# Kernel tuning notes

Measured on AMD Instinct MI355X. Metric: run time of the kernel, lower is better.

## Reference

```python
import jax, jax.numpy as jnp
import numpy as np

T1 = -0.075410217
T2 = 0.0
T3 = 0.062207676


def my_squash2(s_j):
    # s_j: [B, 1, C, O, 1]; piecewise-linear rescale based on sorted channel-0 magnitudes.
    B, _, C, O, _ = s_j.shape
    f = s_j[:, 0, :, 0, 0]                      # [B, C] first element of each capsule
    order = jnp.argsort(f, axis=1)
    srt = jnp.take_along_axis(f, order, axis=1)  # ascending sort per sample
    i1 = jnp.sum(srt < T1, axis=1, keepdims=True)
    i2 = jnp.sum(srt < T2, axis=1, keepdims=True)
    i3 = jnp.sum(srt < T3, axis=1, keepdims=True)
    pos = jnp.arange(C)[None, :]
    seg1 = -0.074520095 * srt + 0.349297946
    seg2 = -0.534473989 * srt + 0.27196494
    seg3 = 0.637642944 * srt + 0.295330779
    seg4 = 0.169344703 * srt + 0.353784456
    # faithful to torch slices [0:i1-1], [i1:i2-1], [i2:i3-1], [i3:9] (segment-end indices untouched)
    m1 = (i1 > 0) & (pos < i1 - 1)
    m2 = (i2 > 0) & (i2 > i1) & (pos >= i1) & (pos < i2 - 1)
    m3 = (i3 > 0) & (i3 > i2) & (pos >= i2) & (pos < i3 - 1)
    m4 = (i3 < C) & (pos >= i3) & (pos < C - 1)
    new_srt = jnp.where(m1, seg1, jnp.where(m2, seg2, jnp.where(m3, seg3, jnp.where(m4, seg4, srt))))
    inv = jnp.argsort(order, axis=1)
    new_f = jnp.take_along_axis(new_srt, inv, axis=1)  # unsort back to capsule order
    # torch code mutates s_j in place: channel 0 of each capsule becomes new_f
    s_mut = s_j.at[:, 0, :, 0, 0].set(new_f)
    scale = new_f[:, None, :, None, None]            # expanded over out_channels
    return scale * s_mut, s_mut


def setup_inputs() -> dict:
    key = jax.random.key(0)
    k0, k1, k2, k3 = jax.random.split(key, 4)
    B, R, C, O, I = 100, 1152, 10, 16, 8
    return {
        "x0": jax.random.normal(k0, (B, R, I), dtype=jnp.float32),
        "x1": jax.random.normal(k1, (B, R, I), dtype=jnp.float32),
        "x2": jax.random.normal(k2, (B, 1, 28, 28), dtype=jnp.float32),
        "W": jax.random.normal(k3, (1, R, C, O, I), dtype=jnp.float32),
        "train_or_test": 0,
        "epch": 0,
    }


def reference(x0, x1, x2, W, train_or_test, epch):
    B, R, I = x0.shape
    C, O = W.shape[2], W.shape[3]
    squashed_u = jnp.broadcast_to(x0[:, :, None, :, None], (B, R, C, I, 1))
    # u_hat[b,r,c,o] = sum_i W[0,r,c,o,i] * x0[b,r,i]
    u_hat = jnp.einsum('rcoi,bri->brco', W[0], x0)[..., None]  # [B,R,C,O,1]
    b_ij = jnp.zeros((1, R, C, 1), dtype=x0.dtype)
    num_iterations = 3
    for it in range(num_iterations):
        c_ij = jax.nn.softmax(b_ij, axis=1)                    # over routes
        c_full = jnp.broadcast_to(c_ij, (B, R, C, 1))[..., None]
        s_j = jnp.sum(c_full * u_hat, axis=1, keepdims=True)   # [B,1,C,O,1]
        v_j, s_mut = my_squash2(s_j)
        if it < num_iterations - 1:
            a = jnp.einsum('brco,bco->brc', u_hat[..., 0], v_j[:, 0, :, :, 0])
            b_ij = b_ij + jnp.mean(a, axis=0)[None, :, :, None]
    Wb = jnp.broadcast_to(W, (B,) + W.shape[1:])
    return (v_j[:, 0], c_full, Wb, squashed_u, x1, x2, s_mut[:, 0])
```

## Files before the change

### kernel.cpp

```cpp
#include <hip/hip_runtime.h>

#define B 100
#define R 1152
#define C 10
#define O 16
#define I 8
#define RI 9216
#define CO 160
#define RCHUNK 32
#define NRC 36
#define KCH (RCHUNK*I)

typedef float f4raw __attribute__((ext_vector_type(4)));
__device__ __forceinline__ void nt_store4(const float4& v, float4* p) {
    __builtin_nontemporal_store(*(const f4raw*)&v, (f4raw*)p);
}

#define WS_BCOL 0
#define WS_CSM  11520
#define WS_XT   23040
#define WS_PART 944768
#define WS_V    1520768
#define WS_SMUT 1536768

#define WB_OUT_BASE 292000
#define WB_WSTRIDE  368640
#define WB_NCHUNK   1440
#define WB_BG       20
#define WB_UNITS    7200

__device__ __forceinline__ void wb_unit(const float4* __restrict__ W4,
                                        float4* __restrict__ out, int unit) {
    int wchunk = unit % WB_NCHUNK;
    int bg = unit / WB_NCHUNK;
    int idx = wchunk * 256 + threadIdx.x;
    float4 v = W4[idx];
    float4* dst = out + WB_OUT_BASE + (size_t)bg * WB_BG * WB_WSTRIDE + idx;
    #pragma unroll
    for (int b = 0; b < WB_BG; b++) {
        nt_store4(v, dst);
        dst += WB_WSTRIDE;
    }
}

__global__ void k_init(const float* __restrict__ x0, float* __restrict__ ws,
                       const float4* __restrict__ W4, float4* __restrict__ out) {
    if (blockIdx.x >= 3600) { wb_unit(W4, out, 0 + (blockIdx.x - 3600)); return; }
    int idx = blockIdx.x * 256 + threadIdx.x;
    if (idx < RI * B) {
        int k = idx / B;
        int b = idx - k * B;
        ws[WS_XT + idx] = x0[b * RI + k];
    }
    if (idx < R * C) ws[WS_BCOL + idx] = 0.f;
}

__global__ __launch_bounds__(256) void k_gemm1(const float* __restrict__ Wg,
                                               float* __restrict__ ws,
                                               float4* __restrict__ out, int wbBase) {
    if (blockIdx.x >= NRC) {
        wb_unit((const float4*)Wg, out, wbBase + (blockIdx.x - NRC) + 90 * blockIdx.y);
        return;
    }
    const int rc = blockIdx.x, c = blockIdx.y;
    const int t = threadIdx.x;
    const int r0 = rc * RCHUNK;
    __shared__ float red[256];
    __shared__ float cw[RCHUNK];
    __shared__ float lw[KCH * O];
    const float* bcol = ws + WS_BCOL + c * R;

    float lm = -3.4e38f;
    for (int r = t; r < R; r += 256) lm = fmaxf(lm, bcol[r]);
    red[t] = lm; __syncthreads();
    for (int s = 128; s > 0; s >>= 1) { if (t < s) red[t] = fmaxf(red[t], red[t + s]); __syncthreads(); }
    const float m = red[0]; __syncthreads();
    float ls = 0.f;
    for (int r = t; r < R; r += 256) ls += expf(bcol[r] - m);
    red[t] = ls; __syncthreads();
    for (int s = 128; s > 0; s >>= 1) { if (t < s) red[t] += red[t + s]; __syncthreads(); }
    const float sinv = 1.f / red[0];
    if (t < RCHUNK) {
        float w_ = expf(bcol[r0 + t] - m) * sinv;
        cw[t] = w_;
        ws[WS_CSM + (r0 + t) * C + c] = w_;
    }
    __syncthreads();

    for (int j = t; j < KCH * O; j += 256) {
        int rr = j >> 7;
        int rem = j & 127;
        int o = rem >> 3, i = rem & 7;
        lw[(rr * I + i) * O + o] = cw[rr] * Wg[((size_t)(r0 + rr) * C + c) * (O * I) + rem];
    }
    __syncthreads();

    const int bl = t & 63, og = t >> 6;
    const float* xT = ws + WS_XT + (r0 * I) * B + bl;
    const float4* lw4 = (const float4*)lw;
    float4 a0 = {0, 0, 0, 0}, a1 = {0, 0, 0, 0};
    #pragma unroll 8
    for (int k = 0; k < KCH; k++) {
        float xv0 = xT[0];
        float xv1 = xT[64];
        float4 wv = lw4[k * 4 + og];
        a0.x += xv0 * wv.x; a0.y += xv0 * wv.y; a0.z += xv0 * wv.z; a0.w += xv0 * wv.w;
        a1.x += xv1 * wv.x; a1.y += xv1 * wv.y; a1.z += xv1 * wv.z; a1.w += xv1 * wv.w;
        xT += B;
    }
    float4* part4 = (float4*)(ws + WS_PART);
    int base = ((c * NRC + rc) * B + bl) * 4 + og;
    part4[base] = a0;
    if (bl < B - 64) part4[base + 64 * 4] = a1;
}

__global__ __launch_bounds__(256) void k_squash(float* __restrict__ ws,
                                                const float4* __restrict__ W4,
                                                float4* __restrict__ out, int wbBase) {
    if (blockIdx.x >= B) { wb_unit(W4, out, wbBase + (blockIdx.x - B)); return; }
    const int b = blockIdx.x, t = threadIdx.x;
    __shared__ float sl[CO];
    __shared__ float nf[C];
    if (t < CO) {
        int c = t >> 4, o = t & 15;
        float s = 0.f;
        const float* p = ws + WS_PART + ((size_t)c * NRC * B + b) * 16 + o;
        #pragma unroll
        for (int rc = 0; rc < NRC; rc++) s += p[(size_t)rc * B * 16];
        sl[t] = s;
    }
    __syncthreads();
    if (t < C) {
        float fv[C];
        #pragma unroll
        for (int c2 = 0; c2 < C; c2++) fv[c2] = sl[c2 * O];
        float mine = sl[t * O];
        int rank = 0, i1 = 0, i2 = 0, i3 = 0;
        #pragma unroll
        for (int c2 = 0; c2 < C; c2++) {
            rank += (fv[c2] < mine) || (fv[c2] == mine && c2 < t);
            i1 += fv[c2] < -0.075410217f;
            i2 += fv[c2] < 0.0f;
            i3 += fv[c2] < 0.062207676f;
        }
        float nv = mine;
        if (i1 > 0 && rank < i1 - 1)                               nv = -0.074520095f * mine + 0.349297946f;
        else if (i2 > 0 && i2 > i1 && rank >= i1 && rank < i2 - 1) nv = -0.534473989f * mine + 0.27196494f;
        else if (i3 > 0 && i3 > i2 && rank >= i2 && rank < i3 - 1) nv = 0.637642944f * mine + 0.295330779f;
        else if (i3 < C && rank >= i3 && rank < C - 1)             nv = 0.169344703f * mine + 0.353784456f;
        nf[t] = nv;
    }
    __syncthreads();
    if (t < CO) {
        int c = t >> 4, o = t & 15;
        float sv = sl[t];
        float nfv = nf[c];
        float smut = (o == 0) ? nfv : sv;
        ws[WS_SMUT + b * CO + t] = smut;
        ws[WS_V + b * CO + t] = nfv * smut;
    }
}

__global__ __launch_bounds__(256) void k_agree(const float* __restrict__ Wg,
                                               float* __restrict__ ws,
                                               float4* __restrict__ out, int wbBase) {
    if (blockIdx.x >= R) { wb_unit((const float4*)Wg, out, wbBase + (blockIdx.x - R)); return; }
    const int r = blockIdx.x, t = threadIdx.x;
    __shared__ float vt[32 * B];
    __shared__ float xs[I * B];
    __shared__ float arr[CO * I];
    for (int j = t; j < I * B; j += 256) xs[j] = ws[WS_XT + (size_t)r * I * B + j];
    const int i = t & 7, co0 = t >> 3;
    const float4* xs4 = (const float4*)(xs + i * B);
    const float4* vt4 = (const float4*)(vt + co0 * B);
    for (int ch = 0; ch < 5; ch++) {
        __syncthreads();
        for (int j = t; j < 32 * B; j += 256) {
            int b = j >> 5, cc = j & 31;
            vt[cc * B + b] = ws[WS_V + b * CO + ch * 32 + cc];
        }
        __syncthreads();
        float q = 0.f;
        #pragma unroll
        for (int b4 = 0; b4 < B / 4; b4++) {
            float4 xv = xs4[b4];
            float4 vv = vt4[b4];
            q += xv.x * vv.x + xv.y * vv.y + xv.z * vv.z + xv.w * vv.w;
        }
        int co = ch * 32 + co0;
        arr[co * I + i] = q * Wg[(size_t)r * (C * O * I) + co * I + i];
    }
    __syncthreads();
    if (t < C) {
        const float4* a4 = (const float4*)(arr + t * 128);
        float d = 0.f;
        #pragma unroll
        for (int m2 = 0; m2 < 32; m2++) { float4 v4 = a4[m2]; d += v4.x + v4.y + v4.z + v4.w; }
        ws[WS_BCOL + t * R + r] += d * (1.0f / B);
    }
}

#define KOUT_BLOCKS 2048
__global__ void k_out(const float* __restrict__ x0, const float* __restrict__ x1,
                      const float* __restrict__ x2, const float* __restrict__ ws,
                      const float4* __restrict__ W4, float4* __restrict__ out,
                      int wbBase) {
    if (blockIdx.x >= KOUT_BLOCKS) { wb_unit(W4, out, wbBase + (blockIdx.x - KOUT_BLOCKS)); return; }
    const float4* x04 = (const float4*)x0;
    const float4* x14 = (const float4*)x1;
    const float4* x24 = (const float4*)x2;
    const float4* v4  = (const float4*)(ws + WS_V);
    const float4* sm4 = (const float4*)(ws + WS_SMUT);
    const float4* cs4 = (const float4*)(ws + WS_CSM);
    const int stride = KOUT_BLOCKS * 256;
    for (int u = blockIdx.x * 256 + threadIdx.x; u < 2850000; u += stride) {
        int g = (u < 292000) ? u : u + 36864000;
        float4 val;
        if (g >= 37156000 && g < 39460000) {
            int j = g - 37156000;
            int br = j / 20;
            val = x04[br * 2 + (j & 1)];
        } else if (g >= 4000 && g < 292000) {
            int j = g - 4000;
            val = cs4[j % 2880];
        } else if (g < 4000) {
            val = v4[g];
        } else if (g < 39690400) {
            val = x14[g - 39460000];
        } else if (g < 39710000) {
            val = x24[g - 39690400];
        } else {
            val = sm4[g - 39710000];
        }
        nt_store4(val, &out[g]);
    }
}

extern "C" void kernel_launch(void* const* d_in, const int* in_sizes, int n_in,
                              void* d_out, int out_size, void* d_ws, size_t ws_size,
                              hipStream_t stream) {
    (void)in_sizes; (void)n_in; (void)out_size; (void)ws_size;
    const float* x0 = (const float*)d_in[0];
    const float* x1 = (const float*)d_in[1];
    const float* x2 = (const float*)d_in[2];
    const float* Wg = (const float*)d_in[3];
    const float4* W4 = (const float4*)Wg;
    float* ws = (float*)d_ws;
    float4* out = (float4*)d_out;

    hipLaunchKernelGGL(k_init, dim3(3600 + 600), dim3(256), 0, stream, x0, ws, W4, out);
    for (int it = 0; it < 3; it++) {
        hipLaunchKernelGGL(k_gemm1, dim3(NRC + 90, C), dim3(256), 0, stream,
                           Wg, ws, out, 600 + 900 * it);
        hipLaunchKernelGGL(k_squash, dim3(B + 500), dim3(256), 0, stream,
                           ws, W4, out, 3300 + 500 * it);
        if (it < 2)
            hipLaunchKernelGGL(k_agree, dim3(R + 700), dim3(256), 0, stream,
                               Wg, ws, out, 4800 + 700 * it);
    }
    hipLaunchKernelGGL(k_out, dim3(KOUT_BLOCKS + 1000), dim3(256), 0, stream,
                       x0, x1, x2, ws, W4, out, 6200);
}
```

Baseline: 234.8 us.

## Fuse squash into agree/output, atomically reduce s_j, use dynamic work queue for W broadcast

Removes the separate squash kernels. s_j is accumulated directly through float atomics in the GEMM kernel, and the squash is recomputed where it is needed, in agree and in the output kernel. The W broadcast writes are handed out through a global atomic work counter, so any block can pick up units instead of following a fixed static assignment. Other changes: the first iteration skips the softmax, c_ij is written only in the last iteration, and x0 is transposed through shared memory. The cost is float atomic contention and nondeterministic summation order, redundant squash recomputation, and an extra memset.

```diff
diff --git a/kernel.cpp b/kernel.cpp
--- a/kernel.cpp
+++ b/kernel.cpp
@@ -6,22 +6,24 @@
 #define O 16
 #define I 8
 #define RI 9216
-#define CO 160
 #define RCHUNK 32
 #define NRC 36
 #define KCH (RCHUNK*I)
 
+#define T1c (-0.075410217f)
+#define T3c (0.062207676f)
+
 typedef float f4raw __attribute__((ext_vector_type(4)));
 __device__ __forceinline__ void nt_store4(const float4& v, float4* p) {
     __builtin_nontemporal_store(*(const f4raw*)&v, (f4raw*)p);
 }
 
-#define WS_BCOL 0
-#define WS_CSM  11520
-#define WS_XT   23040
-#define WS_PART 944768
-#define WS_V    1520768
-#define WS_SMUT 1536768
+#define WS_Q    0
+#define WS_SJ   64
+#define WS_BCOL 48128
+#define WS_CSM  59648
+#define WS_XT   103232
+#define MEMSET_BYTES ((WS_SJ + 48000) * 4)
 
 #define WB_OUT_BASE 292000
 #define WB_WSTRIDE  368640
@@ -37,53 +39,91 @@
     float4 v = W4[idx];
     float4* dst = out + WB_OUT_BASE + (size_t)bg * WB_BG * WB_WSTRIDE + idx;
     #pragma unroll
-    for (int b = 0; b < WB_BG; b++) {
-        nt_store4(v, dst);
-        dst += WB_WSTRIDE;
-    }
-}
-
-__global__ void k_init(const float* __restrict__ x0, float* __restrict__ ws,
-                       const float4* __restrict__ W4, float4* __restrict__ out) {
-    if (blockIdx.x >= 3600) { wb_unit(W4, out, 0 + (blockIdx.x - 3600)); return; }
-    int idx = blockIdx.x * 256 + threadIdx.x;
-    if (idx < RI * B) {
-        int k = idx / B;
-        int b = idx - k * B;
-        ws[WS_XT + idx] = x0[b * RI + k];
-    }
-    if (idx < R * C) ws[WS_BCOL + idx] = 0.f;
-}
-
-__global__ __launch_bounds__(256) void k_gemm1(const float* __restrict__ Wg,
-                                               float* __restrict__ ws,
-                                               float4* __restrict__ out, int wbBase) {
-    if (blockIdx.x >= NRC) {
-        wb_unit((const float4*)Wg, out, wbBase + (blockIdx.x - NRC) + 90 * blockIdx.y);
-        return;
-    }
-    const int rc = blockIdx.x, c = blockIdx.y;
+    for (int b = 0; b < WB_BG; b++) { nt_store4(v, dst); dst += WB_WSTRIDE; }
+}
+
+__device__ __forceinline__ void rider(float* ws, const float4* __restrict__ W4,
+                                      float4* __restrict__ out, int cap) {
+    __shared__ unsigned su;
+    unsigned* q = (unsigned*)ws;
+    for (int n = 0; n < cap; n++) {
+        if (threadIdx.x == 0) su = atomicAdd(q, 1u);
+        __syncthreads();
+        unsigned u = su;
+        __syncthreads();
+        if (u >= WB_UNITS) return;
+        wb_unit(W4, out, u);
+    }
+}
+
+__device__ __forceinline__ float squash_nf(const float* fbase, int stride, int c, int b) {
+    float mine = fbase[(c * 100 + b) * stride];
+    int rank = 0, i1 = 0, i2 = 0, i3 = 0;
+    #pragma unroll
+    for (int c2 = 0; c2 < C; c2++) {
+        float f2 = fbase[(c2 * 100 + b) * stride];
+        rank += (f2 < mine) || (f2 == mine && c2 < c);
+        i1 += f2 < T1c;
+        i2 += f2 < 0.0f;
+        i3 += f2 < T3c;
+    }
+    float nv = mine;
+    if (i1 > 0 && rank < i1 - 1)                               nv = -0.074520095f * mine + 0.349297946f;
+    else if (i2 > 0 && i2 > i1 && rank >= i1 && rank < i2 - 1) nv = -0.534473989f * mine + 0.27196494f;
+    else if (i3 > 0 && i3 > i2 && rank >= i2 && rank < i3 - 1) nv = 0.637642944f * mine + 0.295330779f;
+    else if (i3 < C && rank >= i3 && rank < C - 1)             nv = 0.169344703f * mine + 0.353784456f;
+    return nv;
+}
+
+__global__ __launch_bounds__(256) void k_init(const float* __restrict__ x0,
+                                              float* __restrict__ ws,
+                                              const float4* __restrict__ W4,
+                                              float4* __restrict__ out) {
+    if (blockIdx.x >= 288) { rider(ws, W4, out, 2); return; }
+    __shared__ float tp[32][105];
     const int t = threadIdx.x;
+    const int k0 = blockIdx.x * 32;
+    for (int e = t; e < 3200; e += 256) {
+        int b = e >> 5, kk = e & 31;
+        tp[kk][b] = x0[(size_t)b * RI + k0 + kk];
+    }
+    __syncthreads();
+    for (int e = t; e < 3200; e += 256) {
+        int kk = e / 100, b = e - kk * 100;
+        ws[WS_XT + (size_t)(k0 + kk) * B + b] = tp[kk][b];
+    }
+}
+
+__global__ __launch_bounds__(256) void k_gemm(const float* __restrict__ Wg,
+                                              float* __restrict__ ws,
+                                              float4* __restrict__ out, int it) {
+    const int t = threadIdx.x;
+    if (blockIdx.x >= 360) { rider(ws, (const float4*)Wg, out, 2); return; }
+    const int rc = blockIdx.x % NRC, c = blockIdx.x / NRC;
     const int r0 = rc * RCHUNK;
     __shared__ float red[256];
     __shared__ float cw[RCHUNK];
-    __shared__ float lw[KCH * O];
-    const float* bcol = ws + WS_BCOL + c * R;
-
-    float lm = -3.4e38f;
-    for (int r = t; r < R; r += 256) lm = fmaxf(lm, bcol[r]);
-    red[t] = lm; __syncthreads();
-    for (int s = 128; s > 0; s >>= 1) { if (t < s) red[t] = fmaxf(red[t], red[t + s]); __syncthreads(); }
-    const float m = red[0]; __syncthreads();
-    float ls = 0.f;
-    for (int r = t; r < R; r += 256) ls += expf(bcol[r] - m);
-    red[t] = ls; __syncthreads();
-    for (int s = 128; s > 0; s >>= 1) { if (t < s) red[t] += red[t + s]; __syncthreads(); }
-    const float sinv = 1.f / red[0];
-    if (t < RCHUNK) {
-        float w_ = expf(bcol[r0 + t] - m) * sinv;
-        cw[t] = w_;
-        ws[WS_CSM + (r0 + t) * C + c] = w_;
+    __shared__ __align__(16) float lw[KCH * O];
+
+    if (it > 0) {
+        const float* bcol = ws + WS_BCOL + c * R;
+        float lm = -3.4e38f;
+        for (int r = t; r < R; r += 256) lm = fmaxf(lm, bcol[r]);
+        red[t] = lm; __syncthreads();
+        for (int s = 128; s > 0; s >>= 1) { if (t < s) red[t] = fmaxf(red[t], red[t + s]); __syncthreads(); }
+        const float m = red[0]; __syncthreads();
+        float ls = 0.f;
+        for (int r = t; r < R; r += 256) ls += expf(bcol[r] - m);
+        red[t] = ls; __syncthreads();
+        for (int s = 128; s > 0; s >>= 1) { if (t < s) red[t] += red[t + s]; __syncthreads(); }
+        const float sinv = 1.f / red[0];
+        if (t < RCHUNK) cw[t] = expf(bcol[r0 + t] - m) * sinv;
+        if (it == 2 && rc == 0) {
+            for (int r = t; r < R; r += 256)
+                ws[WS_CSM + r * C + c] = expf(bcol[r] - m) * sinv;
+        }
+    } else {
+        if (t < RCHUNK) cw[t] = 1.0f / 1152.0f;
     }
     __syncthreads();
 
@@ -91,7 +131,7 @@
         int rr = j >> 7;
         int rem = j & 127;
         int o = rem >> 3, i = rem & 7;
-        lw[(rr * I + i) * O + o] = cw[rr] * Wg[((size_t)(r0 + rr) * C + c) * (O * I) + rem];
+        lw[(rr * I + i) * O + o] = cw[rr] * Wg[((size_t)(r0 + rr) * C + c) * 128 + rem];
     }
     __syncthreads();
 
@@ -108,76 +148,48 @@
         a1.x += xv1 * wv.x; a1.y += xv1 * wv.y; a1.z += xv1 * wv.z; a1.w += xv1 * wv.w;
         xT += B;
     }
-    float4* part4 = (float4*)(ws + WS_PART);
-    int base = ((c * NRC + rc) * B + bl) * 4 + og;
-    part4[base] = a0;
-    if (bl < B - 64) part4[base + 64 * 4] = a1;
-}
-
-__global__ __launch_bounds__(256) void k_squash(float* __restrict__ ws,
-                                                const float4* __restrict__ W4,
-                                                float4* __restrict__ out, int wbBase) {
-    if (blockIdx.x >= B) { wb_unit(W4, out, wbBase + (blockIdx.x - B)); return; }
-    const int b = blockIdx.x, t = threadIdx.x;
-    __shared__ float sl[CO];
-    __shared__ float nf[C];
-    if (t < CO) {
-        int c = t >> 4, o = t & 15;
-        float s = 0.f;
-        const float* p = ws + WS_PART + ((size_t)c * NRC * B + b) * 16 + o;
-        #pragma unroll
-        for (int rc = 0; rc < NRC; rc++) s += p[(size_t)rc * B * 16];
-        sl[t] = s;
-    }
-    __syncthreads();
-    if (t < C) {
-        float fv[C];
-        #pragma unroll
-        for (int c2 = 0; c2 < C; c2++) fv[c2] = sl[c2 * O];
-        float mine = sl[t * O];
-        int rank = 0, i1 = 0, i2 = 0, i3 = 0;
-        #pragma unroll
-        for (int c2 = 0; c2 < C; c2++) {
-            rank += (fv[c2] < mine) || (fv[c2] == mine && c2 < t);
-            i1 += fv[c2] < -0.075410217f;
-            i2 += fv[c2] < 0.0f;
-            i3 += fv[c2] < 0.062207676f;
-        }
-        float nv = mine;
-        if (i1 > 0 && rank < i1 - 1)                               nv = -0.074520095f * mine + 0.349297946f;
-        else if (i2 > 0 && i2 > i1 && rank >= i1 && rank < i2 - 1) nv = -0.534473989f * mine + 0.27196494f;
-        else if (i3 > 0 && i3 > i2 && rank >= i2 && rank < i3 - 1) nv = 0.637642944f * mine + 0.295330779f;
-        else if (i3 < C && rank >= i3 && rank < C - 1)             nv = 0.169344703f * mine + 0.353784456f;
-        nf[t] = nv;
-    }
-    __syncthreads();
-    if (t < CO) {
-        int c = t >> 4, o = t & 15;
-        float sv = sl[t];
-        float nfv = nf[c];
-        float smut = (o == 0) ? nfv : sv;
-        ws[WS_SMUT + b * CO + t] = smut;
-        ws[WS_V + b * CO + t] = nfv * smut;
+    float* sj = ws + WS_SJ + it * 16000;
+    int base = (c * B + bl) * O + og * 4;
+    atomicAdd(&sj[base + 0], a0.x); atomicAdd(&sj[base + 1], a0.y);
+    atomicAdd(&sj[base + 2], a0.z); atomicAdd(&sj[base + 3], a0.w);
+    if (bl < B - 64) {
+        int b2 = base + 64 * O;
+        atomicAdd(&sj[b2 + 0], a1.x); atomicAdd(&sj[b2 + 1], a1.y);
+        atomicAdd(&sj[b2 + 2], a1.z); atomicAdd(&sj[b2 + 3], a1.w);
     }
 }
 
 __global__ __launch_bounds__(256) void k_agree(const float* __restrict__ Wg,
                                                float* __restrict__ ws,
-                                               float4* __restrict__ out, int wbBase) {
-    if (blockIdx.x >= R) { wb_unit((const float4*)Wg, out, wbBase + (blockIdx.x - R)); return; }
-    const int r = blockIdx.x, t = threadIdx.x;
-    __shared__ float vt[32 * B];
-    __shared__ float xs[I * B];
-    __shared__ float arr[CO * I];
-    for (int j = t; j < I * B; j += 256) xs[j] = ws[WS_XT + (size_t)r * I * B + j];
+                                               float4* __restrict__ out, int it) {
+    const int t = threadIdx.x;
+    if (blockIdx.x >= R) { rider(ws, (const float4*)Wg, out, 2); return; }
+    const int r = blockIdx.x;
+    __shared__ __align__(16) float vt[3200];
+    __shared__ __align__(16) float xs[800];
+    __shared__ __align__(16) float arr[1280];
+    __shared__ float fs[1000];
+    __shared__ float nfs[1000];
+    const float* sj = ws + WS_SJ + it * 16000;
+
+    for (int j = t; j < 800; j += 256) xs[j] = ws[WS_XT + (size_t)r * 800 + j];
+    for (int j = t; j < 1000; j += 256) fs[j] = sj[j * 16];
+    __syncthreads();
+    for (int j = t; j < 1000; j += 256) nfs[j] = squash_nf(fs, 1, j / 100, j % 100);
+    __syncthreads();
+
     const int i = t & 7, co0 = t >> 3;
     const float4* xs4 = (const float4*)(xs + i * B);
     const float4* vt4 = (const float4*)(vt + co0 * B);
     for (int ch = 0; ch < 5; ch++) {
-        __syncthreads();
-        for (int j = t; j < 32 * B; j += 256) {
+        if (ch) __syncthreads();
+        for (int j = t; j < 3200; j += 256) {
             int b = j >> 5, cc = j & 31;
-            vt[cc * B + b] = ws[WS_V + b * CO + ch * 32 + cc];
+            int co = ch * 32 + cc, c2 = co >> 4, o = co & 15;
+            int cb = c2 * 100 + b;
+            float nfv = nfs[cb];
+            float sv = sj[cb * 16 + o];
+            vt[cc * B + b] = nfv * ((o == 0) ? nfv : sv);
         }
         __syncthreads();
         float q = 0.f;
@@ -188,7 +200,7 @@
             q += xv.x * vv.x + xv.y * vv.y + xv.z * vv.z + xv.w * vv.w;
         }
         int co = ch * 32 + co0;
-        arr[co * I + i] = q * Wg[(size_t)r * (C * O * I) + co * I + i];
+        arr[co * I + i] = q * Wg[(size_t)r * 1280 + co * I + i];
     }
     __syncthreads();
     if (t < C) {
@@ -196,44 +208,55 @@
         float d = 0.f;
         #pragma unroll
         for (int m2 = 0; m2 < 32; m2++) { float4 v4 = a4[m2]; d += v4.x + v4.y + v4.z + v4.w; }
-        ws[WS_BCOL + t * R + r] += d * (1.0f / B);
-    }
-}
-
-#define KOUT_BLOCKS 2048
-__global__ void k_out(const float* __restrict__ x0, const float* __restrict__ x1,
-                      const float* __restrict__ x2, const float* __restrict__ ws,
-                      const float4* __restrict__ W4, float4* __restrict__ out,
-                      int wbBase) {
-    if (blockIdx.x >= KOUT_BLOCKS) { wb_unit(W4, out, wbBase + (blockIdx.x - KOUT_BLOCKS)); return; }
+        float* dst = ws + WS_BCOL + t * R + r;
+        float val = d * (1.0f / B);
+        if (it == 0) *dst = val; else *dst += val;
+    }
+}
+
+#define OUT_BLOCKS 2400
+__global__ __launch_bounds__(256) void k_out(const float* __restrict__ x0,
+                                             const float* __restrict__ x1,
+                                             const float* __restrict__ x2,
+                                             float* __restrict__ ws,
+                                             const float4* __restrict__ W4,
+                                             float4* __restrict__ out) {
     const float4* x04 = (const float4*)x0;
     const float4* x14 = (const float4*)x1;
     const float4* x24 = (const float4*)x2;
-    const float4* v4  = (const float4*)(ws + WS_V);
-    const float4* sm4 = (const float4*)(ws + WS_SMUT);
     const float4* cs4 = (const float4*)(ws + WS_CSM);
-    const int stride = KOUT_BLOCKS * 256;
+    const float* sj2 = ws + WS_SJ + 2 * 16000;
+    const int stride = OUT_BLOCKS * 256;
     for (int u = blockIdx.x * 256 + threadIdx.x; u < 2850000; u += stride) {
         int g = (u < 292000) ? u : u + 36864000;
         float4 val;
         if (g >= 37156000 && g < 39460000) {
             int j = g - 37156000;
-            int br = j / 20;
-            val = x04[br * 2 + (j & 1)];
+            val = x04[(j / 20) * 2 + (j & 1)];
         } else if (g >= 4000 && g < 292000) {
-            int j = g - 4000;
-            val = cs4[j % 2880];
+            val = cs4[(g - 4000) % 2880];
         } else if (g < 4000) {
-            val = v4[g];
+            int fi = g * 4;
+            int b = fi / 160, rem = fi % 160, c = rem >> 4, o = rem & 15;
+            float nf = squash_nf(sj2, 16, c, b);
+            const float* sp = sj2 + (c * 100 + b) * 16 + o;
+            val.x = nf * ((o == 0) ? nf : sp[0]);
+            val.y = nf * sp[1]; val.z = nf * sp[2]; val.w = nf * sp[3];
         } else if (g < 39690400) {
             val = x14[g - 39460000];
         } else if (g < 39710000) {
             val = x24[g - 39690400];
         } else {
-            val = sm4[g - 39710000];
+            int fi = (g - 39710000) * 4;
+            int b = fi / 160, rem = fi % 160, c = rem >> 4, o = rem & 15;
+            float nf = squash_nf(sj2, 16, c, b);
+            const float* sp = sj2 + (c * 100 + b) * 16 + o;
+            val.x = (o == 0) ? nf : sp[0];
+            val.y = sp[1]; val.z = sp[2]; val.w = sp[3];
         }
         nt_store4(val, &out[g]);
     }
+    rider(ws, W4, out, 12);
 }
 
 extern "C" void kernel_launch(void* const* d_in, const int* in_sizes, int n_in,
@@ -248,16 +271,12 @@
     float* ws = (float*)d_ws;
     float4* out = (float4*)d_out;
 
-    hipLaunchKernelGGL(k_init, dim3(3600 + 600), dim3(256), 0, stream, x0, ws, W4, out);
-    for (int it = 0; it < 3; it++) {
-        hipLaunchKernelGGL(k_gemm1, dim3(NRC + 90, C), dim3(256), 0, stream,
-                           Wg, ws, out, 600 + 900 * it);
-        hipLaunchKernelGGL(k_squash, dim3(B + 500), dim3(256), 0, stream,
-                           ws, W4, out, 3300 + 500 * it);
-        if (it < 2)
-            hipLaunchKernelGGL(k_agree, dim3(R + 700), dim3(256), 0, stream,
-                               Wg, ws, out, 4800 + 700 * it);
-    }
-    hipLaunchKernelGGL(k_out, dim3(KOUT_BLOCKS + 1000), dim3(256), 0, stream,
-                       x0, x1, x2, ws, W4, out, 6200);
-}
+    hipMemsetAsync(d_ws, 0, MEMSET_BYTES, stream);
+    hipLaunchKernelGGL(k_init, dim3(288 + 320), dim3(256), 0, stream, x0, ws, W4, out);
+    hipLaunchKernelGGL(k_gemm, dim3(360 + 480), dim3(256), 0, stream, Wg, ws, out, 0);
+    hipLaunchKernelGGL(k_agree, dim3(R + 480), dim3(256), 0, stream, Wg, ws, out, 0);
+    hipLaunchKernelGGL(k_gemm, dim3(360 + 480), dim3(256), 0, stream, Wg, ws, out, 1);
+    hipLaunchKernelGGL(k_agree, dim3(R + 480), dim3(256), 0, stream, Wg, ws, out, 1);
+    hipLaunchKernelGGL(k_gemm, dim3(360 + 480), dim3(256), 0, stream, Wg, ws, out, 2);
+    hipLaunchKernelGGL(k_out, dim3(OUT_BLOCKS), dim3(256), 0, stream, x0, x1, x2, ws, W4, out);
+}
```

After: 340.6 us. +45.0%, slower.
